# Kernel tuning notes

Measured on AMD Instinct MI355X. Metric: run time of the kernel, lower is better.

The kernel has to match this reference:

```python
import jax, jax.numpy as jnp
from jax import lax
import numpy as np

NUM_FRAMES = 16
DIM = 100
BATCH = 65536


def setup_inputs() -> dict:
    key = jax.random.key(0)
    ks = jax.random.split(key, 7)
    s = 1.0 / np.sqrt(DIM)
    return {
        "x": jax.random.normal(ks[0], (BATCH, DIM), dtype=jnp.float32),
        "W0": jax.random.normal(ks[1], (DIM, DIM), dtype=jnp.float32) * s,
        "b0": jax.random.normal(ks[2], (DIM,), dtype=jnp.float32) * 0.01,
        "W1": jax.random.normal(ks[3], (DIM, DIM), dtype=jnp.float32) * s,
        "b1": jax.random.normal(ks[4], (DIM,), dtype=jnp.float32) * 0.01,
        "W_ode": jax.random.normal(ks[5], (DIM, DIM), dtype=jnp.float32) * s,
        "b_ode": jax.random.normal(ks[6], (DIM,), dtype=jnp.float32) * 0.01,
    }


def reference(x, W0, b0, W1, b1, W_ode, b_ode):
    # dsdt encoders -> tuple state (s0, s1), each [B, DIM]
    s0 = x @ W0.T + b0
    s1 = x @ W1.T + b1

    def f(y):  # NOODEFunc: dy0/dt = tanh(Linear(y0)); dy1/dt = y0
        y0, y1 = y
        return (jnp.tanh(y0 @ W_ode.T + b_ode), y0)

    def rk4_step(carry, dt):
        # torchdiffeq 'rk4' fixed-grid solver uses the 3/8-rule variant
        y0, y1 = carry
        k1 = f((y0, y1))
        k2 = f((y0 + dt * k1[0] / 3, y1 + dt * k1[1] / 3))
        k3 = f((y0 + dt * (k2[0] - k1[0] / 3), y1 + dt * (k2[1] - k1[1] / 3)))
        k4 = f((y0 + dt * (k1[0] - k2[0] + k3[0]), y1 + dt * (k1[1] - k2[1] + k3[1])))
        c = dt * 0.125
        ny0 = y0 + c * (k1[0] + 3 * (k2[0] + k3[0]) + k4[0])
        ny1 = y1 + c * (k1[1] + 3 * (k2[1] + k3[1]) + k4[1])
        return (ny0, ny1), ny1  # only the last tuple component is returned

    t = jnp.linspace(0.0, 1.0, NUM_FRAMES, dtype=jnp.float32)
    dts = jnp.diff(t)  # [T-1]
    _, traj = lax.scan(rk4_step, (s0, s1), dts)  # traj: [T-1, B, DIM]
    out = jnp.concatenate([s1[None], traj], axis=0)  # [T, B, DIM]
    return jnp.transpose(out, (1, 0, 2))  # [B, T, DIM]
```

## Files before the change

kernel.cpp:

```cpp
#include <hip/hip_runtime.h>

#define BATCH 65536
#define NF 16

typedef __bf16 bf16;
typedef bf16 bf16x8 __attribute__((ext_vector_type(8)));
typedef float f32x4 __attribute__((ext_vector_type(4)));

__device__ __forceinline__ float tanh_fast(float v) {
  float e = exp2f(v * 2.8853900817779268f);
  return 1.0f - 2.0f * __builtin_amdgcn_rcpf(e + 1.0f);
}

__global__ __launch_bounds__(256) void node_kernel(
    const float* __restrict__ x,
    const float* __restrict__ W0, const float* __restrict__ b0,
    const float* __restrict__ W1, const float* __restrict__ b1,
    const float* __restrict__ Wode, const float* __restrict__ bode,
    float* __restrict__ out)
{
  __shared__ __align__(16) bf16 Au[2][4224];

  const int tid  = threadIdx.x;
  const int lane = tid & 63;
  const int w    = tid >> 6;
  const int col  = lane & 15;
  const int quad = lane >> 4;
  const int rowBase = blockIdx.x * 32;

  const float dt  = 1.0f / 15.0f;
  const float dt3 = dt / 3.0f;
  const float e8  = dt * 0.125f;
  const float q8  = dt * dt * 0.125f;

  const int scat = (col & 1) + (((col >> 2) & 3) << 1) + (((col >> 1) & 1) << 3);
  const int roff[4] = {0, 8, 64, 72};

  int  n[2], abase[2], obase[2];
  bool nok[2];
#pragma unroll
  for (int n2 = 0; n2 < 2; ++n2) {
    n[n2] = (w * 2 + n2) * 16 + col;
    nok[n2] = (n[n2] < 100);
    abase[n2] = ((n[n2] >> 3) * 33 + quad * 2) * 8 + (n[n2] & 7);
    obase[n2] = (rowBase + quad * 4) * (NF * 100) + n[n2];
  }

  bf16x8 bfo[2][4];
  f32x4  bvo[2];
#pragma unroll
  for (int n2 = 0; n2 < 2; ++n2) {
    const float bs = nok[n2] ? bode[n[n2]] : 0.0f;
    bvo[n2] = f32x4{bs, bs, bs, bs};
#pragma unroll
    for (int kc = 0; kc < 4; ++kc)
#pragma unroll
      for (int j = 0; j < 8; ++j) {
        const int k = kc * 32 + quad * 8 + j;
        bfo[n2][kc][j] = (nok[n2] && k < 100) ? (bf16)Wode[n[n2] * 100 + k] : (bf16)0.0f;
      }
  }

#pragma unroll 1
  for (int i = tid; i < 4096; i += 256) {
    const int r32 = i >> 7;
    const int c   = i & 127;
    const float v = (c < 100) ? x[(rowBase + r32) * 100 + c] : 0.0f;
    const int p = (r32 & 16) + (r32 & 1) + (((r32 >> 2) & 3) << 1) + (((r32 >> 1) & 1) << 3);
    Au[0][((c >> 3) * 33 + p) * 8 + (c & 7)] = (bf16)v;
  }

  f32x4 y0a[2][2], y1a[2][2], k1[2][2], k2[2][2];

  {
    bf16x8 bf0[2][4], bf1[2][4];
    float bias0[2], bias1[2];
#pragma unroll
    for (int n2 = 0; n2 < 2; ++n2) {
      bias0[n2] = nok[n2] ? b0[n[n2]] : 0.0f;
      bias1[n2] = nok[n2] ? b1[n[n2]] : 0.0f;
#pragma unroll
      for (int kc = 0; kc < 4; ++kc)
#pragma unroll
        for (int j = 0; j < 8; ++j) {
          const int k = kc * 32 + quad * 8 + j;
          const bool ok = (nok[n2] && k < 100);
          bf0[n2][kc][j] = ok ? (bf16)W0[n[n2] * 100 + k] : (bf16)0.0f;
          bf1[n2][kc][j] = ok ? (bf16)W1[n[n2] * 100 + k] : (bf16)0.0f;
        }
    }

    __syncthreads();

#pragma unroll
    for (int rt = 0; rt < 2; ++rt) {
      bf16x8 af[4];
#pragma unroll
      for (int kc = 0; kc < 4; ++kc)
        af[kc] = *(const bf16x8*)&Au[0][((kc * 4 + quad) * 33 + rt * 16 + scat) * 8];
#pragma unroll
      for (int n2 = 0; n2 < 2; ++n2) {
        f32x4 a0 = { bias0[n2], bias0[n2], bias0[n2], bias0[n2] };
        f32x4 a1 = { bias1[n2], bias1[n2], bias1[n2], bias1[n2] };
#pragma unroll
        for (int kc = 0; kc < 4; ++kc) {
          a0 = __builtin_amdgcn_mfma_f32_16x16x32_bf16(af[kc], bf0[n2][kc], a0, 0, 0, 0);
          a1 = __builtin_amdgcn_mfma_f32_16x16x32_bf16(af[kc], bf1[n2][kc], a1, 0, 0, 0);
        }
        y0a[rt][n2] = a0;
        y1a[rt][n2] = a1;
#pragma unroll
        for (int r = 0; r < 4; ++r) {
          Au[1][abase[n2] + rt * 128 + roff[r]] = (bf16)a0[r];
          if (nok[n2]) out[obase[n2] + rt * 25600 + r * 1600] = a1[r];
        }
      }
    }
  }
  __syncthreads();

#define GEVAL(RD, WR, ...) do {                                                 \
    _Pragma("unroll")                                                           \
    for (int rt = 0; rt < 2; ++rt) {                                            \
      bf16x8 af[4];                                                             \
      _Pragma("unroll")                                                         \
      for (int kc = 0; kc < 4; ++kc)                                            \
        af[kc] = *(const bf16x8*)&Au[RD][((kc * 4 + quad) * 33 + rt * 16 + scat) * 8]; \
      _Pragma("unroll")                                                         \
      for (int n2 = 0; n2 < 2; ++n2) {                                          \
        f32x4 acc = bvo[n2];                                                    \
        _Pragma("unroll")                                                       \
        for (int kc = 0; kc < 4; ++kc)                                          \
          acc = __builtin_amdgcn_mfma_f32_16x16x32_bf16(af[kc], bfo[n2][kc],    \
                                                        acc, 0, 0, 0);          \
        f32x4 z;                                                                \
        _Pragma("unroll")                                                       \
        for (int r = 0; r < 4; ++r) z[r] = tanh_fast(acc[r]);                   \
        f32x4 uw;                                                               \
        __VA_ARGS__;                                                            \
        _Pragma("unroll")                                                       \
        for (int r = 0; r < 4; ++r)                                             \
          Au[WR][abase[n2] + rt * 128 + roff[r]] = (bf16)uw[r];                 \
      }                                                                         \
    }                                                                           \
    __syncthreads();                                                            \
  } while (0)

#pragma unroll 1
  for (int t = 1; t < NF; ++t) {
    const int ot = t * 100;

    GEVAL(1, 0, {
      k1[rt][n2] = z;
      uw = y0a[rt][n2] + dt3 * z;
    });

    GEVAL(0, 1, {
      k2[rt][n2] = z;
      uw = y0a[rt][n2] + dt * z - dt3 * k1[rt][n2];
    });

    GEVAL(1, 0, {
      const f32x4 a   = k1[rt][n2];
      const f32x4 b2  = k2[rt][n2];
      const f32x4 y0v = y0a[rt][n2];
      uw = y0v + dt * (a - b2 + z);
      const f32x4 ny1 = y1a[rt][n2] + dt * y0v + q8 * (a + 2.0f * b2 + z);
      y1a[rt][n2] = ny1;
      y0a[rt][n2] = y0v + e8 * (a + 3.0f * (b2 + z));
      _Pragma("unroll")
      for (int r = 0; r < 4; ++r)
        if (nok[n2]) out[obase[n2] + rt * 25600 + r * 1600 + ot] = ny1[r];
    });

    GEVAL(0, 1, {
      const f32x4 y0v = y0a[rt][n2] + e8 * z;
      y0a[rt][n2] = y0v;
      uw = y0v;
    });
  }
#undef GEVAL
}

extern "C" void kernel_launch(void* const* d_in, const int* in_sizes, int n_in,
                              void* d_out, int out_size, void* d_ws, size_t ws_size,
                              hipStream_t stream) {
  (void)in_sizes; (void)n_in; (void)out_size; (void)d_ws; (void)ws_size;
  const float* x    = (const float*)d_in[0];
  const float* W0   = (const float*)d_in[1];
  const float* b0   = (const float*)d_in[2];
  const float* W1   = (const float*)d_in[3];
  const float* b1   = (const float*)d_in[4];
  const float* Wode = (const float*)d_in[5];
  const float* bode = (const float*)d_in[6];
  float* out = (float*)d_out;

  dim3 grid(BATCH / 32), block(256);
  hipLaunchKernelGGL(node_kernel, grid, block, 0, stream,
                     x, W0, b0, W1, b1, Wode, bode, out);
}
```

Measured before the change: 767.5 us.

## Halve rows per block, store k1/k2 in bf16, and fold tanh scale into weights

Each block now handles 16 rows instead of 32, so the grid doubles, per-thread register state halves and shared memory shrinks. The launch bound asks for 5 blocks per CU. The RK stage values k1 and k2 are kept as bf16 in registers to save VGPRs. The tanh scale constant is pre-multiplied into the ODE weights and bias, removing one multiply per element. The cost is less MFMA work between barriers, Wode weights reloaded by twice as many blocks, and lower precision for k1/k2.

Result: slower. 1.208 ms (+57.5%).

```diff
diff --git a/kernel.cpp b/kernel.cpp
--- a/kernel.cpp
+++ b/kernel.cpp
@@ -4,30 +4,39 @@
 #define NF 16
 
 typedef __bf16 bf16;
+typedef bf16 bf16x4 __attribute__((ext_vector_type(4)));
 typedef bf16 bf16x8 __attribute__((ext_vector_type(8)));
 typedef float f32x4 __attribute__((ext_vector_type(4)));
 
-__device__ __forceinline__ float tanh_fast(float v) {
-  float e = exp2f(v * 2.8853900817779268f);
+__device__ __forceinline__ float tanh_ps(float s) {
+  float e = exp2f(s);
   return 1.0f - 2.0f * __builtin_amdgcn_rcpf(e + 1.0f);
 }
 
-__global__ __launch_bounds__(256) void node_kernel(
+__device__ __forceinline__ bf16x4 cvt4(f32x4 v) {
+  return bf16x4{(bf16)v[0], (bf16)v[1], (bf16)v[2], (bf16)v[3]};
+}
+__device__ __forceinline__ f32x4 up4(bf16x4 v) {
+  return f32x4{(float)v[0], (float)v[1], (float)v[2], (float)v[3]};
+}
+
+__global__ __launch_bounds__(256, 5) void node_kernel(
     const float* __restrict__ x,
     const float* __restrict__ W0, const float* __restrict__ b0,
     const float* __restrict__ W1, const float* __restrict__ b1,
     const float* __restrict__ Wode, const float* __restrict__ bode,
     float* __restrict__ out)
 {
-  __shared__ __align__(16) bf16 Au[2][4224];
+  __shared__ __align__(16) bf16 Au[2][2176];
 
   const int tid  = threadIdx.x;
   const int lane = tid & 63;
   const int w    = tid >> 6;
   const int col  = lane & 15;
   const int quad = lane >> 4;
-  const int rowBase = blockIdx.x * 32;
-
+  const int rowBase = blockIdx.x * 16;
+
+  const float C   = 2.8853900817779268f;
   const float dt  = 1.0f / 15.0f;
   const float dt3 = dt / 3.0f;
   const float e8  = dt * 0.125f;
@@ -42,35 +51,36 @@
   for (int n2 = 0; n2 < 2; ++n2) {
     n[n2] = (w * 2 + n2) * 16 + col;
     nok[n2] = (n[n2] < 100);
-    abase[n2] = ((n[n2] >> 3) * 33 + quad * 2) * 8 + (n[n2] & 7);
+    abase[n2] = ((n[n2] >> 3) * 17 + quad * 2) * 8 + (n[n2] & 7);
     obase[n2] = (rowBase + quad * 4) * (NF * 100) + n[n2];
   }
 
   bf16x8 bfo[2][4];
-  f32x4  bvo[2];
+  float  biaso[2];
 #pragma unroll
   for (int n2 = 0; n2 < 2; ++n2) {
-    const float bs = nok[n2] ? bode[n[n2]] : 0.0f;
-    bvo[n2] = f32x4{bs, bs, bs, bs};
+    biaso[n2] = nok[n2] ? bode[n[n2]] * C : 0.0f;
 #pragma unroll
     for (int kc = 0; kc < 4; ++kc)
 #pragma unroll
       for (int j = 0; j < 8; ++j) {
         const int k = kc * 32 + quad * 8 + j;
-        bfo[n2][kc][j] = (nok[n2] && k < 100) ? (bf16)Wode[n[n2] * 100 + k] : (bf16)0.0f;
+        bfo[n2][kc][j] = (nok[n2] && k < 100) ? (bf16)(Wode[n[n2] * 100 + k] * C)
+                                              : (bf16)0.0f;
       }
   }
 
 #pragma unroll 1
-  for (int i = tid; i < 4096; i += 256) {
-    const int r32 = i >> 7;
+  for (int i = tid; i < 2048; i += 256) {
+    const int r16 = i >> 7;
     const int c   = i & 127;
-    const float v = (c < 100) ? x[(rowBase + r32) * 100 + c] : 0.0f;
-    const int p = (r32 & 16) + (r32 & 1) + (((r32 >> 2) & 3) << 1) + (((r32 >> 1) & 1) << 3);
-    Au[0][((c >> 3) * 33 + p) * 8 + (c & 7)] = (bf16)v;
-  }
-
-  f32x4 y0a[2][2], y1a[2][2], k1[2][2], k2[2][2];
+    const float v = (c < 100) ? x[(rowBase + r16) * 100 + c] : 0.0f;
+    const int p = (r16 & 1) + (((r16 >> 2) & 3) << 1) + (((r16 >> 1) & 1) << 3);
+    Au[0][((c >> 3) * 17 + p) * 8 + (c & 7)] = (bf16)v;
+  }
+
+  f32x4  y0a[2], y1a[2];
+  bf16x4 k1[2], k2[2];
 
   {
     bf16x8 bf0[2][4], bf1[2][4];
@@ -92,56 +102,50 @@
 
     __syncthreads();
 
-#pragma unroll
-    for (int rt = 0; rt < 2; ++rt) {
-      bf16x8 af[4];
-#pragma unroll
-      for (int kc = 0; kc < 4; ++kc)
-        af[kc] = *(const bf16x8*)&Au[0][((kc * 4 + quad) * 33 + rt * 16 + scat) * 8];
-#pragma unroll
-      for (int n2 = 0; n2 < 2; ++n2) {
-        f32x4 a0 = { bias0[n2], bias0[n2], bias0[n2], bias0[n2] };
-        f32x4 a1 = { bias1[n2], bias1[n2], bias1[n2], bias1[n2] };
-#pragma unroll
-        for (int kc = 0; kc < 4; ++kc) {
-          a0 = __builtin_amdgcn_mfma_f32_16x16x32_bf16(af[kc], bf0[n2][kc], a0, 0, 0, 0);
-          a1 = __builtin_amdgcn_mfma_f32_16x16x32_bf16(af[kc], bf1[n2][kc], a1, 0, 0, 0);
-        }
-        y0a[rt][n2] = a0;
-        y1a[rt][n2] = a1;
-#pragma unroll
-        for (int r = 0; r < 4; ++r) {
-          Au[1][abase[n2] + rt * 128 + roff[r]] = (bf16)a0[r];
-          if (nok[n2]) out[obase[n2] + rt * 25600 + r * 1600] = a1[r];
-        }
+    bf16x8 af[4];
+#pragma unroll
+    for (int kc = 0; kc < 4; ++kc)
+      af[kc] = *(const bf16x8*)&Au[0][((kc * 4 + quad) * 17 + scat) * 8];
+#pragma unroll
+    for (int n2 = 0; n2 < 2; ++n2) {
+      f32x4 a0 = { bias0[n2], bias0[n2], bias0[n2], bias0[n2] };
+      f32x4 a1 = { bias1[n2], bias1[n2], bias1[n2], bias1[n2] };
+#pragma unroll
+      for (int kc = 0; kc < 4; ++kc) {
+        a0 = __builtin_amdgcn_mfma_f32_16x16x32_bf16(af[kc], bf0[n2][kc], a0, 0, 0, 0);
+        a1 = __builtin_amdgcn_mfma_f32_16x16x32_bf16(af[kc], bf1[n2][kc], a1, 0, 0, 0);
+      }
+      y0a[n2] = a0;
+      y1a[n2] = a1;
+#pragma unroll
+      for (int r = 0; r < 4; ++r) {
+        Au[1][abase[n2] + roff[r]] = (bf16)a0[r];
+        if (nok[n2]) out[obase[n2] + r * 1600] = a1[r];
       }
     }
   }
   __syncthreads();
 
 #define GEVAL(RD, WR, ...) do {                                                 \
+    bf16x8 af[4];                                                               \
     _Pragma("unroll")                                                           \
-    for (int rt = 0; rt < 2; ++rt) {                                            \
-      bf16x8 af[4];                                                             \
+    for (int kc = 0; kc < 4; ++kc)                                              \
+      af[kc] = *(const bf16x8*)&Au[RD][((kc * 4 + quad) * 17 + scat) * 8];      \
+    _Pragma("unroll")                                                           \
+    for (int n2 = 0; n2 < 2; ++n2) {                                            \
+      f32x4 acc = { biaso[n2], biaso[n2], biaso[n2], biaso[n2] };               \
       _Pragma("unroll")                                                         \
       for (int kc = 0; kc < 4; ++kc)                                            \
-        af[kc] = *(const bf16x8*)&Au[RD][((kc * 4 + quad) * 33 + rt * 16 + scat) * 8]; \
+        acc = __builtin_amdgcn_mfma_f32_16x16x32_bf16(af[kc], bfo[n2][kc],      \
+                                                      acc, 0, 0, 0);            \
+      f32x4 z;                                                                  \
       _Pragma("unroll")                                                         \
-      for (int n2 = 0; n2 < 2; ++n2) {                                          \
-        f32x4 acc = bvo[n2];                                                    \
-        _Pragma("unroll")                                                       \
-        for (int kc = 0; kc < 4; ++kc)                                          \
-          acc = __builtin_amdgcn_mfma_f32_16x16x32_bf16(af[kc], bfo[n2][kc],    \
-                                                        acc, 0, 0, 0);          \
-        f32x4 z;                                                                \
-        _Pragma("unroll")                                                       \
-        for (int r = 0; r < 4; ++r) z[r] = tanh_fast(acc[r]);                   \
-        f32x4 uw;                                                               \
-        __VA_ARGS__;                                                            \
-        _Pragma("unroll")                                                       \
-        for (int r = 0; r < 4; ++r)                                             \
-          Au[WR][abase[n2] + rt * 128 + roff[r]] = (bf16)uw[r];                 \
-      }                                                                         \
+      for (int r = 0; r < 4; ++r) z[r] = tanh_ps(acc[r]);                       \
+      f32x4 uw;                                                                 \
+      __VA_ARGS__;                                                              \
+      _Pragma("unroll")                                                         \
+      for (int r = 0; r < 4; ++r)                                               \
+        Au[WR][abase[n2] + roff[r]] = (bf16)uw[r];                              \
     }                                                                           \
     __syncthreads();                                                            \
   } while (0)
@@ -151,31 +155,31 @@
     const int ot = t * 100;
 
     GEVAL(1, 0, {
-      k1[rt][n2] = z;
-      uw = y0a[rt][n2] + dt3 * z;
+      k1[n2] = cvt4(z);
+      uw = y0a[n2] + dt3 * z;
     });
 
     GEVAL(0, 1, {
-      k2[rt][n2] = z;
-      uw = y0a[rt][n2] + dt * z - dt3 * k1[rt][n2];
+      k2[n2] = cvt4(z);
+      uw = y0a[n2] + dt * z - dt3 * up4(k1[n2]);
     });
 
     GEVAL(1, 0, {
-      const f32x4 a   = k1[rt][n2];
-      const f32x4 b2  = k2[rt][n2];
-      const f32x4 y0v = y0a[rt][n2];
+      const f32x4 a   = up4(k1[n2]);
+      const f32x4 b2  = up4(k2[n2]);
+      const f32x4 y0v = y0a[n2];
       uw = y0v + dt * (a - b2 + z);
-      const f32x4 ny1 = y1a[rt][n2] + dt * y0v + q8 * (a + 2.0f * b2 + z);
-      y1a[rt][n2] = ny1;
-      y0a[rt][n2] = y0v + e8 * (a + 3.0f * (b2 + z));
+      const f32x4 ny1 = y1a[n2] + dt * y0v + q8 * (a + 2.0f * b2 + z);
+      y1a[n2] = ny1;
+      y0a[n2] = y0v + e8 * (a + 3.0f * (b2 + z));
       _Pragma("unroll")
       for (int r = 0; r < 4; ++r)
-        if (nok[n2]) out[obase[n2] + rt * 25600 + r * 1600 + ot] = ny1[r];
+        if (nok[n2]) out[obase[n2] + r * 1600 + ot] = ny1[r];
     });
 
     GEVAL(0, 1, {
-      const f32x4 y0v = y0a[rt][n2] + e8 * z;
-      y0a[rt][n2] = y0v;
+      const f32x4 y0v = y0a[n2] + e8 * z;
+      y0a[n2] = y0v;
       uw = y0v;
     });
   }
@@ -195,7 +199,7 @@
   const float* bode = (const float*)d_in[6];
   float* out = (float*)d_out;
 
-  dim3 grid(BATCH / 32), block(256);
+  dim3 grid(BATCH / 16), block(256);
   hipLaunchKernelGGL(node_kernel, grid, block, 0, stream,
                      x, W0, b0, W1, b1, Wode, bode, out);
 }
```
